# Kernel optimization log

Hardware: AMD Instinct MI355X
Metric: run time of the kernel (lower is better)

The kernel has to match this reference:

```python
import jax, jax.numpy as jnp
import numpy as np

EPS = 1e-5

def conv(x, w, groups=1):
    # x: NCHW, w: OIHW, VALID padding, stride 1 (cross-correlation, same as torch conv2d)
    return jax.lax.conv_general_dilated(x, w, (1, 1), 'VALID',
                                        feature_group_count=groups,
                                        dimension_numbers=('NCHW', 'OIHW', 'NCHW'))

def bn(x, g, b, m, v):
    # eval-mode batchnorm with running stats
    scale = (g / jnp.sqrt(v + EPS))[None, :, None, None]
    return (x - m[None, :, None, None]) * scale + b[None, :, None, None]

def xcorr_depthwise(x, k):
    # x: [B,C,Hs,Ws] search, k: [B,C,Hk,Wk] per-sample kernels
    B, C, H, W = x.shape
    xr = x.reshape(1, B * C, H, W)
    kr = k.reshape(B * C, 1, k.shape[2], k.shape[3])
    out = conv(xr, kr, groups=B * C)  # [1, B*C, Ho, Wo]
    return out.reshape(B, C, out.shape[2], out.shape[3])

def setup_inputs() -> dict:
    key = jax.random.key(0)
    ks = jax.random.split(key, 16)
    Cin, Hid, Cout = 256, 256, 20
    inp = {
        'kernel': jax.random.normal(ks[0], (128, Cin, 7, 7), jnp.float32),
        'search': jax.random.normal(ks[1], (128, Cin, 31, 31), jnp.float32),
        'wk': jax.random.normal(ks[2], (Hid, Cin, 3, 3), jnp.float32) * 0.02,
        'gk': jnp.ones((Hid,), jnp.float32),
        'bk': jnp.zeros((Hid,), jnp.float32),
        'mk': jax.random.normal(ks[3], (Hid,), jnp.float32) * 0.1,
        'vk': jax.random.uniform(ks[4], (Hid,), jnp.float32) + 0.5,
        'ws': jax.random.normal(ks[5], (Hid, Cin, 3, 3), jnp.float32) * 0.02,
        'gs': jnp.ones((Hid,), jnp.float32),
        'bs': jnp.zeros((Hid,), jnp.float32),
        'ms': jax.random.normal(ks[6], (Hid,), jnp.float32) * 0.1,
        'vs': jax.random.uniform(ks[7], (Hid,), jnp.float32) + 0.5,
        'wh1': jax.random.normal(ks[8], (Hid, Hid, 1, 1), jnp.float32) * 0.02,
        'gh': jnp.ones((Hid,), jnp.float32),
        'bh': jnp.zeros((Hid,), jnp.float32),
        'mh': jax.random.normal(ks[9], (Hid,), jnp.float32) * 0.1,
        'vh': jax.random.uniform(ks[10], (Hid,), jnp.float32) + 0.5,
        'wh2': jax.random.normal(ks[11], (Cout, Hid, 1, 1), jnp.float32) * 0.02,
        'bh2': jnp.zeros((Cout,), jnp.float32),
    }
    return inp

def reference(kernel, search, wk, gk, bk, mk, vk, ws, gs, bs, ms, vs,
              wh1, gh, bh, mh, vh, wh2, bh2):
    k = jax.nn.relu(bn(conv(kernel, wk), gk, bk, mk, vk))   # [B,256,5,5]
    s = jax.nn.relu(bn(conv(search, ws), gs, bs, ms, vs))   # [B,256,29,29]
    f = xcorr_depthwise(s, k)                               # [B,256,25,25]
    h = jax.nn.relu(bn(conv(f, wh1), gh, bh, mh, vh))
    out = conv(h, wh2) + bh2[None, :, None, None]           # [B,20,25,25]
    return out
```

## Files before the change

kernel.cpp:

```cpp
#include <hip/hip_runtime.h>

typedef __bf16 bf16x8 __attribute__((ext_vector_type(8)));
typedef float floatx4 __attribute__((ext_vector_type(4)));
typedef unsigned short u16;
typedef unsigned int u32;

__device__ __forceinline__ u16 f2bf(float f) {
    union { float f; unsigned int u; } q; q.f = f;
    unsigned int r = q.u + 0x7FFFu + ((q.u >> 16) & 1u);
    return (u16)(r >> 16);
}
__device__ __forceinline__ float bf2f(u16 b) {
    union { unsigned int u; float f; } q; q.u = ((unsigned int)b) << 16;
    return q.f;
}

__device__ __forceinline__ void gl2lds16(const u16* g, u16* l) {
    __builtin_amdgcn_global_load_lds((const __attribute__((address_space(1))) u32*)g,
                                     (__attribute__((address_space(3))) u32*)l, 16, 0, 0);
}

__global__ __launch_bounds__(256) void prep_all(
    const float* __restrict__ wk, const float* __restrict__ wsw, const float* __restrict__ wh1,
    const float* __restrict__ gk, const float* __restrict__ bk,
    const float* __restrict__ mk, const float* __restrict__ vk,
    const float* __restrict__ gs, const float* __restrict__ bs,
    const float* __restrict__ ms, const float* __restrict__ vs,
    const float* __restrict__ gh, const float* __restrict__ bh,
    const float* __restrict__ mh, const float* __restrict__ vh,
    u16* __restrict__ WKP, u16* __restrict__ WSP, u16* __restrict__ WH1P,
    float* __restrict__ par)
{
    int bid = blockIdx.x, t = threadIdx.x;
    if (bid < 4608) {
        const float* src = (bid < 2304) ? wk : wsw;
        u16* dst = (bid < 2304) ? WKP : WSP;
        int tid = ((bid < 2304) ? bid : bid - 2304) * 256 + t;
        int o  = tid / 2304;
        int k  = tid - o * 2304;
        int rc = k >> 8;
        int ci = k & 255;
        dst[tid] = f2bf(src[o * 2304 + ci * 9 + rc]);
    } else if (bid < 4864) {
        int tid = (bid - 4608) * 256 + t;
        WH1P[tid] = f2bf(wh1[tid]);
    } else {
        float s;
        s = gk[t] * rsqrtf(vk[t] + 1e-5f); par[0*256+t] = s; par[1*256+t] = bk[t] - mk[t]*s;
        s = gs[t] * rsqrtf(vs[t] + 1e-5f); par[2*256+t] = s; par[3*256+t] = bs[t] - ms[t]*s;
        s = gh[t] * rsqrtf(vh[t] + 1e-5f); par[4*256+t] = s; par[5*256+t] = bh[t] - mh[t]*s;
    }
}

__global__ __launch_bounds__(256) void nchw2nhwc_both(
    const float* __restrict__ kin, u16* __restrict__ KIN,
    const float* __restrict__ sin_, u16* __restrict__ SIN)
{
    __shared__ float tile[64][33];
    int bid = blockIdx.x;
    const float* in; u16* out; int HW, sptiles;
    if (bid < 1024) { in = kin;  out = KIN; HW = 49;  sptiles = 2; }
    else { bid -= 1024; in = sin_; out = SIN; HW = 961; sptiles = 31; }
    int st  = bid % sptiles;
    int tmp = bid / sptiles;
    int ct  = tmp & 3;
    int b   = tmp >> 2;
    int sp0 = st * 32, ci0 = ct * 64;
    int t = threadIdx.x;
    int j = t & 31, i8 = t >> 5;
    const float* ip = in + ((size_t)b * 256 + ci0 + i8) * HW + sp0 + j;
#pragma unroll
    for (int k = 0; k < 8; ++k) {
        if (sp0 + j < HW) tile[i8 + k * 8][j] = ip[(size_t)(k * 8) * HW];
    }
    __syncthreads();
    int cl = t & 63, s4 = t >> 6;
#pragma unroll
    for (int k = 0; k < 8; ++k) {
        int spl = s4 + k * 4;
        int sp  = sp0 + spl;
        if (sp < HW) out[((size_t)b * HW + sp) * 256 + ci0 + cl] = f2bf(tile[cl][spl]);
    }
}

#define NS_BLK 421
__global__ __launch_bounds__(512, 2) void conv_gemm256(
    const u16* __restrict__ AinS, const u16* __restrict__ WpkS,
    const float* __restrict__ parS, u16* __restrict__ OutS,
    const u16* __restrict__ AinK, const u16* __restrict__ WpkK,
    const float* __restrict__ parK, u16* __restrict__ OutK)
{
    __shared__ __align__(16) u16 Alds[2][256][64];
    __shared__ __align__(16) u16 Blds[2][256][64];

    const int Ktot = 2304;
    const int NKT  = 36;
    const int KW   = 3;

    const int lid = blockIdx.x;
    const bool isk = (lid >= NS_BLK);

    int nid;
    if (!isk) {
        const int xcd = lid & 7, sub = lid >> 3;
        nid = (xcd < 5) ? (xcd * 53 + sub) : (265 + (xcd - 5) * 52 + sub);
    } else {
        nid = lid - NS_BLK;
    }
    const int m0 = nid << 8;

    const int OHW     = isk ? 25    : 841;
    const int OW      = isk ? 5     : 29;
    const int IW      = isk ? 7     : 31;
    const int bstride = isk ? 12544 : 246016;
    const int Mtot    = isk ? 3200  : 107648;
    const u16* Ain    = isk ? AinK : AinS;
    const u16* Wpk    = isk ? WpkK : WpkS;
    const float* scale = isk ? parK : parS;
    const float* shift = scale + 256;
    u16* Out          = isk ? OutK : OutS;

    const int t     = threadIdx.x;
    const int wave  = t >> 6;
    const int lane  = t & 63;
    const int lrow  = lane & 15;
    const int lquad = lane >> 4;
    const int wmBase = (wave >> 2) << 7;
    const int wnBase = (wave & 3) << 6;

    const u16* pA[4];
    const u16* pB[4];
#pragma unroll
    for (int j = 0; j < 4; ++j) {
        int u = j * 512 + t;
        int row = u >> 3, slot = u & 7;
        int ko = ((slot ^ (row & 7)) << 3);
        int m = m0 + row; if (m >= Mtot) m = Mtot - 1;
        int b = m / OHW; int rem = m - b * OHW; int y = rem / OW; int x = rem - y * OW;
        pA[j] = Ain + (size_t)b * bstride + (size_t)(y * IW + x) * 256 + ko;
        pB[j] = Wpk + (size_t)row * (size_t)Ktot + ko;
    }

    const int xo0 = ((lquad ^ (lrow & 7)) << 3);
    const int xo1 = xo0 ^ 32;

    floatx4 acc[8][4];
#pragma unroll
    for (int i = 0; i < 8; ++i)
#pragma unroll
        for (int j = 0; j < 4; ++j) acc[i][j] = (floatx4){0.f, 0.f, 0.f, 0.f};

#pragma unroll
    for (int j = 0; j < 4; ++j)
        gl2lds16(pA[j], &Alds[0][0][0] + j * 4096 + wave * 512);
#pragma unroll
    for (int j = 0; j < 4; ++j)
        gl2lds16(pB[j], &Blds[0][0][0] + j * 4096 + wave * 512);
    asm volatile("s_waitcnt vmcnt(0)" ::: "memory");
    __builtin_amdgcn_s_barrier();

#define LOADA(mb) do {                                              \
        const u16* _p = Ab + (wmBase + (mb) * 16 + lrow) * 64;      \
        aF[0][0] = *(const bf16x8*)(_p + xo0);                      \
        aF[0][1] = *(const bf16x8*)(_p + xo1);                      \
        aF[1][0] = *(const bf16x8*)(_p + 1024 + xo0);               \
        aF[1][1] = *(const bf16x8*)(_p + 1024 + xo1);               \
    } while (0)

#define MFMA16(mb) do {                                                                               \
        _Pragma("unroll")                                                                             \
        for (int _n = 0; _n < 4; ++_n) {                                                              \
            acc[(mb)][_n]     = __builtin_amdgcn_mfma_f32_16x16x32_bf16(aF[0][0], bB[_n][0], acc[(mb)][_n], 0, 0, 0);     \
            acc[(mb)][_n]     = __builtin_amdgcn_mfma_f32_16x16x32_bf16(aF[0][1], bB[_n][1], acc[(mb)][_n], 0, 0, 0);     \
            acc[(mb) + 1][_n] = __builtin_amdgcn_mfma_f32_16x16x32_bf16(aF[1][0], bB[_n][0], acc[(mb) + 1][_n], 0, 0, 0); \
            acc[(mb) + 1][_n] = __builtin_amdgcn_mfma_f32_16x16x32_bf16(aF[1][1], bB[_n][1], acc[(mb) + 1][_n], 0, 0, 0); \
        }                                                                                             \
    } while (0)

#define PH_MID() do {                                        \
        __builtin_amdgcn_s_barrier();                        \
        asm volatile("s_waitcnt lgkmcnt(0)" ::: "memory");   \
        __builtin_amdgcn_s_setprio(1);                       \
    } while (0)

#define PH_END() do {                                        \
        __builtin_amdgcn_s_setprio(0);                       \
        __builtin_amdgcn_s_barrier();                        \
    } while (0)

#pragma unroll 2
    for (int kt = 0; kt < NKT; ++kt) {
        const int c = kt & 1;
        const u16* Ab = &Alds[c][0][0];
        const u16* Bb = &Blds[c][0][0];
        u16* An = &Alds[c ^ 1][0][0];
        u16* Bn = &Blds[c ^ 1][0][0];
        const int pf = (kt + 1 < NKT);
        const int kt1 = kt + 1;
        const int rc = kt1 >> 2;
        const int rr = rc / KW;
        const int cc = rc - rr * KW;
        const int aoffA = (rr * IW + cc) * 256 + ((kt1 & 3) << 6);
        const int boffB = kt1 << 6;

        bf16x8 bB[4][2];
        bf16x8 aF[2][2];

#pragma unroll
        for (int ni = 0; ni < 4; ++ni) {
            const u16* _p = Bb + (wnBase + ni * 16 + lrow) * 64;
            bB[ni][0] = *(const bf16x8*)(_p + xo0);
            bB[ni][1] = *(const bf16x8*)(_p + xo1);
        }
        LOADA(0);
        if (pf) {
#pragma unroll
            for (int j = 0; j < 4; ++j)
                gl2lds16(pA[j] + aoffA, An + j * 4096 + wave * 512);
        }
        PH_MID();
        MFMA16(0);
        PH_END();

        LOADA(2);
        if (pf) {
#pragma unroll
            for (int j = 0; j < 4; ++j)
                gl2lds16(pB[j] + boffB, Bn + j * 4096 + wave * 512);
        }
        PH_MID();
        MFMA16(2);
        PH_END();

        LOADA(4);
        PH_MID();
        MFMA16(4);
        PH_END();

        LOADA(6);
        PH_MID();
        MFMA16(6);
        __builtin_amdgcn_s_setprio(0);
        asm volatile("s_waitcnt vmcnt(0)" ::: "memory");
        __builtin_amdgcn_s_barrier();
    }

#undef LOADA
#undef MFMA16
#undef PH_MID
#undef PH_END

    float sc[4], sh[4];
#pragma unroll
    for (int ni = 0; ni < 4; ++ni) {
        int gn = wnBase + ni * 16 + lrow;
        sc[ni] = scale[gn];
        sh[ni] = shift[gn];
    }
#pragma unroll
    for (int mi = 0; mi < 8; ++mi) {
        int gm0 = m0 + wmBase + mi * 16 + (lquad << 2);
#pragma unroll
        for (int ri = 0; ri < 4; ++ri) {
            int gm = gm0 + ri;
            if (gm < Mtot) {
                size_t ro = (size_t)gm * 256 + wnBase + lrow;
#pragma unroll
                for (int ni = 0; ni < 4; ++ni) {
                    float v = acc[mi][ni][ri] * sc[ni] + sh[ni];
                    v = fmaxf(v, 0.f);
                    Out[ro + ni * 16] = f2bf(v);
                }
            }
        }
    }
}

__global__ __launch_bounds__(256) void xcorr_conv1(
    const u16* __restrict__ ss, const u16* __restrict__ kk,
    const u16* __restrict__ w1, const float* __restrict__ parh,
    u16* __restrict__ hh)
{
    __shared__ __align__(16) u16 Flds[32 * 264];

    int lid = blockIdx.x;
    int bid = (lid & 7) * 400 + (lid >> 3);
    int b = bid / 25, y = bid - b * 25;
    int t = threadIdx.x;

    {
        int cg = (t & 31) << 3;
        int xg = t >> 5;
        const u16* kbase = kk + (size_t)b * 25 * 256 + cg;
        const u16* sbase = ss + (size_t)(b * 29 + y) * 29 * 256 + cg;

        float acc[4][8];
#pragma unroll
        for (int j = 0; j < 4; ++j)
#pragma unroll
            for (int e = 0; e < 8; ++e) acc[j][e] = 0.f;

#pragma unroll
        for (int r = 0; r < 5; ++r) {
            const u16* srow = sbase + (size_t)r * 29 * 256;
#pragma unroll
            for (int c = 0; c < 5; ++c) {
                bf16x8 kv = *(const bf16x8*)(kbase + (r * 5 + c) * 256);
                float kf[8];
#pragma unroll
                for (int e = 0; e < 8; ++e) kf[e] = (float)kv[e];
#pragma unroll
                for (int j = 0; j < 4; ++j) {
                    int x = xg + 8 * j;
                    if (x < 25) {
                        bf16x8 sv = *(const bf16x8*)(srow + (size_t)(x + c) * 256);
#pragma unroll
                        for (int e = 0; e < 8; ++e) acc[j][e] += (float)sv[e] * kf[e];
                    }
                }
            }
        }
#pragma unroll
        for (int j = 0; j < 4; ++j) {
            int x = xg + 8 * j;
            if (x < 25) {
                u16 pk[8];
#pragma unroll
                for (int e = 0; e < 8; ++e) pk[e] = f2bf(acc[j][e]);
                *(bf16x8*)&Flds[x * 264 + cg] = *(const bf16x8*)pk;
            }
        }
    }
    __syncthreads();

    {
        int wave = t >> 6, lane = t & 63;
        int lr = lane & 15, lq = lane >> 4;
        int nb = wave << 6;

        floatx4 hacc[2][4];
#pragma unroll
        for (int i = 0; i < 2; ++i)
#pragma unroll
            for (int j = 0; j < 4; ++j) hacc[i][j] = (floatx4){0.f, 0.f, 0.f, 0.f};

#pragma unroll
        for (int ks = 0; ks < 8; ++ks) {
            int ko = ks * 32 + lq * 8;
            bf16x8 a0 = *(const bf16x8*)&Flds[(lr)      * 264 + ko];
            bf16x8 a1 = *(const bf16x8*)&Flds[(16 + lr) * 264 + ko];
            bf16x8 bv[4];
#pragma unroll
            for (int ni = 0; ni < 4; ++ni)
                bv[ni] = *(const bf16x8*)&w1[(size_t)(nb + ni * 16 + lr) * 256 + ko];
#pragma unroll
            for (int ni = 0; ni < 4; ++ni) {
                hacc[0][ni] = __builtin_amdgcn_mfma_f32_16x16x32_bf16(a0, bv[ni], hacc[0][ni], 0, 0, 0);
                hacc[1][ni] = __builtin_amdgcn_mfma_f32_16x16x32_bf16(a1, bv[ni], hacc[1][ni], 0, 0, 0);
            }
        }

        float sc[4], sh[4];
#pragma unroll
        for (int ni = 0; ni < 4; ++ni) {
            int gn = nb + ni * 16 + lr;
            sc[ni] = parh[gn];
            sh[ni] = parh[256 + gn];
        }
        u16* hrow = hh + (size_t)bid * 25 * 256;
#pragma unroll
        for (int mt = 0; mt < 2; ++mt) {
#pragma unroll
            for (int reg = 0; reg < 4; ++reg) {
                int row = mt * 16 + lq * 4 + reg;
                if (row < 25) {
#pragma unroll
                    for (int ni = 0; ni < 4; ++ni) {
                        float v = hacc[mt][ni][reg] * sc[ni] + sh[ni];
                        v = fmaxf(v, 0.f);
                        hrow[row * 256 + nb + ni * 16 + lr] = f2bf(v);
                    }
                }
            }
        }
    }
}

__global__ __launch_bounds__(256) void head(const u16* __restrict__ h, const float* __restrict__ w2,
                                            const float* __restrict__ b2, float* __restrict__ out) {
    __shared__ __align__(16) u16   hl[25 * 264];
    __shared__ __align__(16) float wl[20 * 260];
    int bid = blockIdx.x;
    int b = bid / 25, y = bid - b * 25;
    int t = threadIdx.x;
    const u16* hrow = h + (size_t)(b * 25 + y) * 25 * 256;
    for (int i = t; i < 800; i += 256) {
        int x = i >> 5, c8 = i & 31;
        *(bf16x8*)&hl[x * 264 + c8 * 8] = *(const bf16x8*)&hrow[i * 8];
    }
    for (int i = t; i < 1280; i += 256) {
        int co = i >> 6, c4 = i & 63;
        *(float4*)&wl[co * 260 + c4 * 4] = *(const float4*)&w2[(size_t)co * 256 + c4 * 4];
    }
    __syncthreads();
    for (int o = t; o < 500; o += 256) {
        int x = o / 20, co = o - x * 20;
        float acc = b2[co];
        const u16* hp = &hl[x * 264];
        const float* wp = &wl[co * 260];
#pragma unroll 4
        for (int k = 0; k < 256; k += 8) {
            bf16x8 hv = *(const bf16x8*)(hp + k);
            float4 w0 = *(const float4*)(wp + k);
            float4 w1v = *(const float4*)(wp + k + 4);
            acc += (float)hv[0] * w0.x + (float)hv[1] * w0.y
                 + (float)hv[2] * w0.z + (float)hv[3] * w0.w
                 + (float)hv[4] * w1v.x + (float)hv[5] * w1v.y
                 + (float)hv[6] * w1v.z + (float)hv[7] * w1v.w;
        }
        out[(size_t)((b * 20 + co) * 25 + y) * 25 + x] = acc;
    }
}

#define OFF_SIN  0ull
#define SZ_SIN   62980096ull
#define OFF_KIN  (OFF_SIN + SZ_SIN)
#define SZ_KIN   3211264ull
#define OFF_WKP  (OFF_KIN + SZ_KIN)
#define SZ_WKP   1179648ull
#define OFF_WSP  (OFF_WKP + SZ_WKP)
#define SZ_WSP   1179648ull
#define OFF_WH1P (OFF_WSP + SZ_WSP)
#define SZ_WH1P  131072ull
#define OFF_PAR  (OFF_WH1P + SZ_WH1P)
#define SZ_PAR   8192ull
#define OFF_KK   (OFF_PAR + SZ_PAR)
#define SZ_KK    1638400ull
#define OFF_SS   (OFF_KK + SZ_KK)
#define SZ_SS    55115776ull
#define OFF_H    OFF_SIN

extern "C" void kernel_launch(void* const* d_in, const int* in_sizes, int n_in,
                              void* d_out, int out_size, void* d_ws, size_t ws_size,
                              hipStream_t stream) {
    const float* kin  = (const float*)d_in[0];
    const float* sin_ = (const float*)d_in[1];
    const float* wk   = (const float*)d_in[2];
    const float* gk   = (const float*)d_in[3];
    const float* bk   = (const float*)d_in[4];
    const float* mk   = (const float*)d_in[5];
    const float* vk   = (const float*)d_in[6];
    const float* wsw  = (const float*)d_in[7];
    const float* gs   = (const float*)d_in[8];
    const float* bs   = (const float*)d_in[9];
    const float* ms   = (const float*)d_in[10];
    const float* vs   = (const float*)d_in[11];
    const float* wh1  = (const float*)d_in[12];
    const float* gh   = (const float*)d_in[13];
    const float* bh   = (const float*)d_in[14];
    const float* mh   = (const float*)d_in[15];
    const float* vh   = (const float*)d_in[16];
    const float* wh2  = (const float*)d_in[17];
    const float* bh2  = (const float*)d_in[18];
    float* out = (float*)d_out;

    char* w = (char*)d_ws;
    u16*   SIN  = (u16*)(w + OFF_SIN);
    u16*   KIN  = (u16*)(w + OFF_KIN);
    u16*   WKP  = (u16*)(w + OFF_WKP);
    u16*   WSP  = (u16*)(w + OFF_WSP);
    u16*   WH1P = (u16*)(w + OFF_WH1P);
    float* PAR  = (float*)(w + OFF_PAR);
    u16*   KK   = (u16*)(w + OFF_KK);
    u16*   SS   = (u16*)(w + OFF_SS);
    u16*   HH   = (u16*)(w + OFF_H);

    prep_all<<<4865, 256, 0, stream>>>(wk, wsw, wh1,
                                       gk, bk, mk, vk, gs, bs, ms, vs, gh, bh, mh, vh,
                                       WKP, WSP, WH1P, PAR);
    nchw2nhwc_both<<<1024 + 15872, 256, 0, stream>>>(kin, KIN, sin_, SIN);

    conv_gemm256<<<434, 512, 0, stream>>>(SIN, WSP, PAR + 512, SS,
                                          KIN, WKP, PAR + 0, KK);
    xcorr_conv1<<<3200, 256, 0, stream>>>(SS, KK, WH1P, PAR + 1024, HH);
    head<<<3200, 256, 0, stream>>>(HH, wh2, bh2, out);

    (void)in_sizes; (void)n_in; (void)out_size; (void)ws_size;
}
```

Before: 547.8 us.

## Fuse the 1x1 head conv into the xcorr+conv1 kernel through LDS

The final 1x1 head convolution now runs inside the xcorr/conv1 kernel. The BN-ReLU'd hidden row is written to the existing LDS tile instead of global memory and read straight back for the 20-channel head dot products. This drops the round trip of the intermediate hidden tensor through HBM and one kernel launch. In exchange, the head weights are read from global/L1 instead of staged in LDS, and an extra barrier plus the serial head loop lengthens each block.

```diff
diff --git a/kernel.cpp b/kernel.cpp
--- a/kernel.cpp
+++ b/kernel.cpp
@@ -276,10 +276,11 @@
     }
 }
 
-__global__ __launch_bounds__(256) void xcorr_conv1(
+__global__ __launch_bounds__(256) void xcorr_head(
     const u16* __restrict__ ss, const u16* __restrict__ kk,
     const u16* __restrict__ w1, const float* __restrict__ parh,
-    u16* __restrict__ hh)
+    const float* __restrict__ w2, const float* __restrict__ b2,
+    float* __restrict__ out)
 {
     __shared__ __align__(16) u16 Flds[32 * 264];
 
@@ -367,7 +368,7 @@
             sc[ni] = parh[gn];
             sh[ni] = parh[256 + gn];
         }
-        u16* hrow = hh + (size_t)bid * 25 * 256;
+        __syncthreads();
 #pragma unroll
         for (int mt = 0; mt < 2; ++mt) {
 #pragma unroll
@@ -378,36 +379,19 @@
                     for (int ni = 0; ni < 4; ++ni) {
                         float v = hacc[mt][ni][reg] * sc[ni] + sh[ni];
                         v = fmaxf(v, 0.f);
-                        hrow[row * 256 + nb + ni * 16 + lr] = f2bf(v);
+                        Flds[row * 264 + nb + ni * 16 + lr] = f2bf(v);
                     }
                 }
             }
         }
     }
-}
-
-__global__ __launch_bounds__(256) void head(const u16* __restrict__ h, const float* __restrict__ w2,
-                                            const float* __restrict__ b2, float* __restrict__ out) {
-    __shared__ __align__(16) u16   hl[25 * 264];
-    __shared__ __align__(16) float wl[20 * 260];
-    int bid = blockIdx.x;
-    int b = bid / 25, y = bid - b * 25;
-    int t = threadIdx.x;
-    const u16* hrow = h + (size_t)(b * 25 + y) * 25 * 256;
-    for (int i = t; i < 800; i += 256) {
-        int x = i >> 5, c8 = i & 31;
-        *(bf16x8*)&hl[x * 264 + c8 * 8] = *(const bf16x8*)&hrow[i * 8];
-    }
-    for (int i = t; i < 1280; i += 256) {
-        int co = i >> 6, c4 = i & 63;
-        *(float4*)&wl[co * 260 + c4 * 4] = *(const float4*)&w2[(size_t)co * 256 + c4 * 4];
-    }
     __syncthreads();
+
     for (int o = t; o < 500; o += 256) {
         int x = o / 20, co = o - x * 20;
         float acc = b2[co];
-        const u16* hp = &hl[x * 264];
-        const float* wp = &wl[co * 260];
+        const u16* hp = &Flds[x * 264];
+        const float* wp = w2 + (size_t)co * 256;
 #pragma unroll 4
         for (int k = 0; k < 256; k += 8) {
             bf16x8 hv = *(const bf16x8*)(hp + k);
@@ -438,7 +422,6 @@
 #define SZ_KK    1638400ull
 #define OFF_SS   (OFF_KK + SZ_KK)
 #define SZ_SS    55115776ull
-#define OFF_H    OFF_SIN
 
 extern "C" void kernel_launch(void* const* d_in, const int* in_sizes, int n_in,
                               void* d_out, int out_size, void* d_ws, size_t ws_size,
@@ -473,7 +456,6 @@
     float* PAR  = (float*)(w + OFF_PAR);
     u16*   KK   = (u16*)(w + OFF_KK);
     u16*   SS   = (u16*)(w + OFF_SS);
-    u16*   HH   = (u16*)(w + OFF_H);
 
     prep_all<<<4865, 256, 0, stream>>>(wk, wsw, wh1,
                                        gk, bk, mk, vk, gs, bs, ms, vs, gh, bh, mh, vh,
@@ -482,8 +464,7 @@
 
     conv_gemm256<<<434, 512, 0, stream>>>(SIN, WSP, PAR + 512, SS,
                                           KIN, WKP, PAR + 0, KK);
-    xcorr_conv1<<<3200, 256, 0, stream>>>(SS, KK, WH1P, PAR + 1024, HH);
-    head<<<3200, 256, 0, stream>>>(HH, wh2, bh2, out);
+    xcorr_head<<<3200, 256, 0, stream>>>(SS, KK, WH1P, PAR + 1024, wh2, bh2, out);
 
     (void)in_sizes; (void)n_in; (void)out_size; (void)ws_size;
 }
```

After: 677.1 us. 1.24x slower.
